# Kernel optimization log

Measured on AMD Instinct MI355X. Metric: run time of the kernel, lower is better.

Reference implementation:

```python
import jax, jax.numpy as jnp
import numpy as np

N = 100_000      # nodes
E = 3_200_000    # edges
H = 32           # hidden_dim
L = 4            # num_layers
G = 1_000        # graphs in batch
F_IN = 1         # num_features
C = 2            # num_classes
BN_EPS = 1e-5


def setup_inputs() -> dict:
    key = jax.random.key(0)
    ks = jax.random.split(key, 8)
    s = 0.1  # param init scale
    x = jax.random.normal(ks[0], (N, F_IN), jnp.float32)
    edge_index = jax.random.randint(ks[1], (2, E), 0, N, dtype=jnp.int64)
    batch = jnp.sort(jax.random.randint(ks[2], (N,), 0, G, dtype=jnp.int64))
    return {
        "x": x,
        "edge_index": edge_index,
        "batch": batch,
        "W_enc": jax.random.normal(ks[3], (F_IN, H), jnp.float32) * s,
        "b_enc": jnp.zeros((H,), jnp.float32),
        "eps": jnp.zeros((L,), jnp.float32),           # GIN train_eps, init 0
        "W1": jax.random.normal(ks[4], (L, H, H), jnp.float32) * s,
        "b1": jnp.zeros((L, H), jnp.float32),
        "W2": jax.random.normal(ks[5], (L, H, H), jnp.float32) * s,
        "b2": jnp.zeros((L, H), jnp.float32),
        "gamma": jnp.ones((L, H), jnp.float32),
        "beta": jnp.zeros((L, H), jnp.float32),
        "W_cls": jax.random.normal(ks[6], (H, C), jnp.float32) * s,
        "b_cls": jnp.zeros((C,), jnp.float32),
    }


def reference(x, edge_index, batch, W_enc, b_enc, eps, W1, b1, W2, b2,
              gamma, beta, W_cls, b_cls):
    h = x @ W_enc + b_enc                      # [N, H] node encoder
    src, dst = edge_index[0], edge_index[1]    # message flow src -> dst
    for l in range(L):
        # GINConv: (1+eps)*x + sum_{j in N(i)} x_j
        agg = jax.ops.segment_sum(h[src], dst, num_segments=N)   # [N, H]
        z = (1.0 + eps[l]) * h + agg
        # 2-layer MLP
        z = jnp.maximum(z @ W1[l] + b1[l], 0.0) @ W2[l] + b2[l]
        # BatchNorm1d (training-mode batch statistics over nodes)
        mu = z.mean(axis=0)
        var = z.var(axis=0)
        z = gamma[l] * (z - mu) * jax.lax.rsqrt(var + BN_EPS) + beta[l]
        h = jnp.maximum(z, 0.0)                # ReLU (dropout = identity, eval)
    pooled = jax.ops.segment_sum(h, batch, num_segments=G)   # global_add_pool
    return pooled @ W_cls + b_cls              # [G, C]
```

## Files before the change

kernel.cpp:

```cpp
#include <hip/hip_runtime.h>

#define N_NODES 100000
#define N_EDGES 3200000
#define HD      32
#define NLAYERS 4
#define NGRAPHS 1000
#define BN_EPS  1e-5f
#define BSHIFT  9
#define NBUCK   ((N_NODES + 511) >> 9)
#define PCHUNK  8192
#define NPB     ((N_EDGES + PCHUNK - 1) / PCHUNK)
#define ZBLOCKS ((NGRAPHS * HD + 255) / 256)

typedef _Float16 f16;
typedef _Float16 f16x8 __attribute__((ext_vector_type(8)));
typedef float    f32x4 __attribute__((ext_vector_type(4)));
typedef int      i32x4 __attribute__((ext_vector_type(4)));
typedef unsigned int  u32x2 __attribute__((ext_vector_type(2)));
typedef unsigned char uc8 __attribute__((ext_vector_type(8)));

__global__ __launch_bounds__(256) void k_encphist(
    const int* __restrict__ ei, float* __restrict__ stats,
    float* __restrict__ pooled, int* __restrict__ pcnt)
{
    __shared__ int hist[256];
    int bb = blockIdx.x, t = threadIdx.x;
    if (bb < NPB) {
        hist[t] = 0;
        __syncthreads();
        int base4 = bb * (PCHUNK / 4);
        int n4 = min(PCHUNK / 4, N_EDGES / 4 - base4);
        const i32x4* d4 = (const i32x4*)(ei + N_EDGES);
        for (int k = t; k < n4; k += 256) {
            i32x4 d = __builtin_nontemporal_load(d4 + base4 + k);
            atomicAdd(&hist[d.x >> BSHIFT], 1);
            atomicAdd(&hist[d.y >> BSHIFT], 1);
            atomicAdd(&hist[d.z >> BSHIFT], 1);
            atomicAdd(&hist[d.w >> BSHIFT], 1);
        }
        __syncthreads();
        pcnt[t * NPB + bb] = hist[t];
    } else {
        int gid = (bb - NPB) * 256 + t;
        if (gid < NLAYERS * 64)   stats[gid]  = 0.f;
        if (gid < NGRAPHS * HD)   pooled[gid] = 0.f;
    }
}

__global__ __launch_bounds__(512) void k_pscanA(int* __restrict__ pcnt,
                                                int* __restrict__ btot)
{
    __shared__ int sc[2][512];
    int t = threadIdx.x, b = blockIdx.x;
    int base = b * NPB;
    int v = (t < NPB) ? pcnt[base + t] : 0;
    int pp = 0;
    sc[0][t] = v;
    __syncthreads();
    for (int st = 1; st < 512; st <<= 1) {
        int x = sc[pp][t];
        if (t >= st) x += sc[pp][t - st];
        sc[pp ^ 1][t] = x;
        pp ^= 1;
        __syncthreads();
    }
    int incl = sc[pp][t];
    if (t < NPB) pcnt[base + t] = incl - v;
    if (t == NPB - 1) btot[b] = incl;
}

__global__ __launch_bounds__(256) void k_pscatter(const int* __restrict__ ei,
                                                  const int* __restrict__ pcnt,
                                                  const int* __restrict__ btot,
                                                  unsigned int* __restrict__ ebuf)
{
    __shared__ int sb[2][256];
    __shared__ int lcur[256];
    int t = threadIdx.x, blk = blockIdx.x;
    sb[0][t] = (t < NBUCK) ? btot[t] : 0;
    __syncthreads();
    int pp = 0;
    for (int st = 1; st < 256; st <<= 1) {
        int v = sb[pp][t];
        if (t >= st) v += sb[pp][t - st];
        sb[pp ^ 1][t] = v;
        pp ^= 1;
        __syncthreads();
    }
    int bexcl = (t == 0) ? 0 : sb[pp][t - 1];
    lcur[t] = pcnt[t * NPB + blk] + bexcl;
    __syncthreads();
    int base4 = blk * (PCHUNK / 4);
    int n4 = min(PCHUNK / 4, N_EDGES / 4 - base4);
    const i32x4* s4 = (const i32x4*)ei;
    const i32x4* d4 = (const i32x4*)(ei + N_EDGES);
    for (int k = t; k < n4; k += 256) {
        i32x4 s = __builtin_nontemporal_load(s4 + base4 + k);
        i32x4 d = __builtin_nontemporal_load(d4 + base4 + k);
        int pos;
        pos = atomicAdd(&lcur[d.x >> BSHIFT], 1);
        ebuf[pos] = ((unsigned)s.x << BSHIFT) | (unsigned)(d.x & 511);
        pos = atomicAdd(&lcur[d.y >> BSHIFT], 1);
        ebuf[pos] = ((unsigned)s.y << BSHIFT) | (unsigned)(d.y & 511);
        pos = atomicAdd(&lcur[d.z >> BSHIFT], 1);
        ebuf[pos] = ((unsigned)s.z << BSHIFT) | (unsigned)(d.z & 511);
        pos = atomicAdd(&lcur[d.w >> BSHIFT], 1);
        ebuf[pos] = ((unsigned)s.w << BSHIFT) | (unsigned)(d.w & 511);
    }
}

__global__ __launch_bounds__(512) void k_bfinal(const unsigned int* __restrict__ ebuf,
                                                const int* __restrict__ btot,
                                                const float* __restrict__ x,
                                                int* __restrict__ off,
                                                int* __restrict__ csr,
                                                float* __restrict__ usum)
{
    __shared__ int sb[2][256];
    __shared__ int cnt[512], scanbuf[2][512], cur[512];
    __shared__ float fsum[512];
    int tid = threadIdx.x, b = blockIdx.x;
    if (tid < 256) sb[0][tid] = (tid < NBUCK) ? btot[tid] : 0;
    fsum[tid] = 0.f;
    __syncthreads();
    int pp = 0;
    for (int st = 1; st < 256; st <<= 1) {
        if (tid < 256) {
            int v = sb[pp][tid];
            if (tid >= st) v += sb[pp][tid - st];
            sb[pp ^ 1][tid] = v;
        }
        pp ^= 1;
        __syncthreads();
    }
    int base = (b == 0) ? 0 : sb[pp][b - 1];
    int nE = sb[pp][b] - base;
    if (b == NBUCK - 1 && tid == 0) off[N_NODES] = sb[pp][NBUCK - 1];
    cnt[tid] = 0;
    __syncthreads();
    for (int e = tid; e < nE; e += 512)
        atomicAdd(&cnt[ebuf[base + e] & 511], 1);
    __syncthreads();
    int p2 = 0;
    scanbuf[0][tid] = cnt[tid];
    __syncthreads();
    for (int st = 1; st < 512; st <<= 1) {
        int v = scanbuf[p2][tid];
        if (tid >= st) v += scanbuf[p2][tid - st];
        scanbuf[p2 ^ 1][tid] = v;
        p2 ^= 1;
        __syncthreads();
    }
    int excl = scanbuf[p2][tid] - cnt[tid];
    cur[tid] = excl;
    int gnode = (b << BSHIFT) + tid;
    if (gnode < N_NODES) off[gnode] = base + excl;
    __syncthreads();
    for (int e = tid; e < nE; e += 512) {
        unsigned int p = ebuf[base + e];
        int src = (int)(p >> BSHIFT);
        int pos = atomicAdd(&cur[p & 511], 1);
        csr[base + pos] = src;
        atomicAdd(&fsum[p & 511], x[src]);
    }
    __syncthreads();
    if (gnode < N_NODES) usum[gnode] = fsum[tid];
}

__global__ __launch_bounds__(256, 6) void k_fused(
    const unsigned char* __restrict__ hq, const float* __restrict__ x,
    const float* __restrict__ usum, const int* __restrict__ off,
    const int* __restrict__ csr, const float* __restrict__ epsArr,
    const float* __restrict__ gamma, const float* __restrict__ beta,
    const float* __restrict__ W_enc, const float* __restrict__ b_enc,
    const float* __restrict__ W1, const float* __restrict__ b1,
    const float* __restrict__ W2, const float* __restrict__ b2,
    f16* __restrict__ z2out, float* __restrict__ stats, int layer)
{
    __shared__ f16 AT[4][16][5][8];
    __shared__ float T[4][16 * 36];
    __shared__ float redS[4][32], redQ[4][32];
    int tid = threadIdx.x, wave = tid >> 6, lane = tid & 63;
    int col = lane & 15, quad = lane >> 4;
    int unit = tid >> 2, li = tid & 3, ul = unit & 15;
    int node = blockIdx.x * 64 + unit;
    bool valid = node < N_NODES;
    int co = li * 8;

    f16x8 r;
    #pragma unroll
    for (int k = 0; k < 8; ++k) r[k] = (f16)0.f;

    if (valid) {
        if (layer == 0) {
            int j0 = off[node], jend = off[node + 1];
            float oneEps = 1.f + epsArr[0];
            float u  = fmaf(oneEps, x[node], usum[node]);
            float dv = oneEps + (float)(jend - j0);
            #pragma unroll
            for (int k = 0; k < 8; ++k)
                r[k] = (f16)(fmaf(u, W_enc[co + k], dv * b_enc[co + k]));
        } else {
            const unsigned MASK = 0x00FF00FFu;
            int j = off[node], jend = off[node + 1];
            u32x2 gs = *(const u32x2*)(hq + (size_t)node * 32 + co);
            unsigned a0 = 0, a1 = 0, a2 = 0, a3 = 0;
            auto accum = [&](u32x2 v) {
                a0 += v.x & MASK; a1 += (v.x >> 8) & MASK;
                a2 += v.y & MASK; a3 += (v.y >> 8) & MASK;
            };
            auto rowp = [&](int idx) {
                return (const u32x2*)(hq + (size_t)idx * 32 + co);
            };
            while (j < jend && (j & 3))
                accum(*rowp(csr[j++]));
            int nrem = jend - j;
            while (nrem >= 16) {
                i32x4 q0 = __builtin_nontemporal_load((const i32x4*)(csr + j));
                i32x4 q1 = __builtin_nontemporal_load((const i32x4*)(csr + j + 4));
                i32x4 q2 = __builtin_nontemporal_load((const i32x4*)(csr + j + 8));
                i32x4 q3 = __builtin_nontemporal_load((const i32x4*)(csr + j + 12));
                u32x2 g0 = *rowp(q0.x), g1 = *rowp(q0.y);
                u32x2 g2 = *rowp(q0.z), g3 = *rowp(q0.w);
                u32x2 g4 = *rowp(q1.x), g5 = *rowp(q1.y);
                u32x2 g6 = *rowp(q1.z), g7 = *rowp(q1.w);
                u32x2 g8 = *rowp(q2.x), g9 = *rowp(q2.y);
                u32x2 gA = *rowp(q2.z), gB = *rowp(q2.w);
                u32x2 gC = *rowp(q3.x), gD = *rowp(q3.y);
                u32x2 gE = *rowp(q3.z), gF = *rowp(q3.w);
                accum(g0); accum(g1); accum(g2); accum(g3);
                accum(g4); accum(g5); accum(g6); accum(g7);
                accum(g8); accum(g9); accum(gA); accum(gB);
                accum(gC); accum(gD); accum(gE); accum(gF);
                j += 16; nrem -= 16;
            }
            if (nrem >= 8) {
                i32x4 q0 = *(const i32x4*)(csr + j);
                i32x4 q1 = *(const i32x4*)(csr + j + 4);
                u32x2 g0 = *rowp(q0.x), g1 = *rowp(q0.y);
                u32x2 g2 = *rowp(q0.z), g3 = *rowp(q0.w);
                u32x2 g4 = *rowp(q1.x), g5 = *rowp(q1.y);
                u32x2 g6 = *rowp(q1.z), g7 = *rowp(q1.w);
                accum(g0); accum(g1); accum(g2); accum(g3);
                accum(g4); accum(g5); accum(g6); accum(g7);
                j += 8; nrem -= 8;
            }
            if (nrem >= 4) {
                i32x4 q0 = *(const i32x4*)(csr + j);
                accum(*rowp(q0.x)); accum(*rowp(q0.y));
                accum(*rowp(q0.z)); accum(*rowp(q0.w));
                j += 4;
            }
            while (j < jend)
                accum(*rowp(csr[j++]));

            float oneEps = 1.f + epsArr[layer];
            float F[8];
            F[0] = (float)(a0 & 0xFFFF); F[2] = (float)(a0 >> 16);
            F[1] = (float)(a1 & 0xFFFF); F[3] = (float)(a1 >> 16);
            F[4] = (float)(a2 & 0xFFFF); F[6] = (float)(a2 >> 16);
            F[5] = (float)(a3 & 0xFFFF); F[7] = (float)(a3 >> 16);
            #pragma unroll
            for (int k = 0; k < 4; ++k) {
                float gLo  = gamma[(layer - 1) * 32 + co + k];
                float bLo  = beta[(layer - 1) * 32 + co + k];
                float gHi  = gamma[(layer - 1) * 32 + co + k + 4];
                float bHi  = beta[(layer - 1) * 32 + co + k + 4];
                float sLo = fmaxf(fmaxf(bLo + 5.5f * fabsf(gLo), 0.f), 1e-6f) / 255.f;
                float sHi = fmaxf(fmaxf(bHi + 5.5f * fabsf(gHi), 0.f), 1e-6f) / 255.f;
                float qsl = (float)((gs.x >> (8 * k)) & 255u);
                float qsh = (float)((gs.y >> (8 * k)) & 255u);
                r[k]     = (f16)(sLo * (F[k]     + oneEps * qsl));
                r[k + 4] = (f16)(sHi * (F[k + 4] + oneEps * qsh));
            }
        }
    }

    if (valid) *(f16x8*)&AT[wave][ul][li][0] = r;

    float sA = 0.f, qA = 0.f, sB = 0.f, qB = 0.f;
    if (valid) {
        f16x8 a = *(const f16x8*)&AT[wave][col][quad][0];
        const float* W1l = W1 + layer * 1024;
        const float* W2l = W2 + layer * 1024;
        f16x8 w1a, w1b, w2a, w2b;
        #pragma unroll
        for (int jj = 0; jj < 8; ++jj) {
            int k = quad * 8 + jj;
            w1a[jj] = (f16)W1l[k * 32 + col];
            w1b[jj] = (f16)W1l[k * 32 + col + 16];
            w2a[jj] = (f16)W2l[k * 32 + col];
            w2b[jj] = (f16)W2l[k * 32 + col + 16];
        }
        float b1a = b1[layer * 32 + col], b1b = b1[layer * 32 + col + 16];
        float b2a = b2[layer * 32 + col], b2b = b2[layer * 32 + col + 16];
        f32x4 bias1a = {b1a, b1a, b1a, b1a}, bias1b = {b1b, b1b, b1b, b1b};
        f32x4 bias2a = {b2a, b2a, b2a, b2a}, bias2b = {b2b, b2b, b2b, b2b};
        float* Tw = T[wave];

        f32x4 m0 = __builtin_amdgcn_mfma_f32_16x16x32_f16(a, w1a, bias1a, 0, 0, 0);
        f32x4 m1 = __builtin_amdgcn_mfma_f32_16x16x32_f16(a, w1b, bias1b, 0, 0, 0);
        #pragma unroll
        for (int rr = 0; rr < 4; ++rr) {
            int row = quad * 4 + rr;
            Tw[row * 36 + col]      = fmaxf(m0[rr], 0.f);
            Tw[row * 36 + col + 16] = fmaxf(m1[rr], 0.f);
        }
        f32x4 t0 = *(const f32x4*)(Tw + col * 36 + quad * 8);
        f32x4 t1 = *(const f32x4*)(Tw + col * 36 + quad * 8 + 4);
        f16x8 a2;
        #pragma unroll
        for (int k = 0; k < 4; ++k) { a2[k] = (f16)t0[k]; a2[k + 4] = (f16)t1[k]; }
        f32x4 z0 = __builtin_amdgcn_mfma_f32_16x16x32_f16(a2, w2a, bias2a, 0, 0, 0);
        f32x4 zb = __builtin_amdgcn_mfma_f32_16x16x32_f16(a2, w2b, bias2b, 0, 0, 0);
        int nb = blockIdx.x * 64 + wave * 16;
        #pragma unroll
        for (int rr = 0; rr < 4; ++rr) {
            int n2 = nb + quad * 4 + rr;
            __builtin_nontemporal_store((f16)z0[rr], z2out + n2 * 32 + col);
            __builtin_nontemporal_store((f16)zb[rr], z2out + n2 * 32 + col + 16);
            sA += z0[rr]; qA += z0[rr] * z0[rr];
            sB += zb[rr]; qB += zb[rr] * zb[rr];
        }
    }

    sA += __shfl_xor(sA, 16); sA += __shfl_xor(sA, 32);
    qA += __shfl_xor(qA, 16); qA += __shfl_xor(qA, 32);
    sB += __shfl_xor(sB, 16); sB += __shfl_xor(sB, 32);
    qB += __shfl_xor(qB, 16); qB += __shfl_xor(qB, 32);
    if (lane < 16) {
        redS[wave][col] = sA; redS[wave][col + 16] = sB;
        redQ[wave][col] = qA; redQ[wave][col + 16] = qB;
    }
    __syncthreads();
    if (tid < 64) {
        int sel = tid >> 5, cc = tid & 31;
        float s = 0.f;
        #pragma unroll
        for (int w = 0; w < 4; ++w) s += sel ? redQ[w][cc] : redS[w][cc];
        atomicAdd(&stats[layer * 64 + sel * 32 + cc], s);
    }
}

__global__ __launch_bounds__(256) void k_quant(
    const f16* __restrict__ z2, const float* __restrict__ stats,
    const float* __restrict__ gamma, const float* __restrict__ beta,
    unsigned char* __restrict__ hq, int layer)
{
    int idx = blockIdx.x * 256 + threadIdx.x;
    if (idx >= N_NODES * 4) return;
    int c0 = (idx & 3) * 8;
    const float invN = 1.0f / (float)N_NODES;
    float bnsc[8], bnsh[8], inv_s[8];
    #pragma unroll
    for (int k = 0; k < 8; ++k) {
        int ch = c0 + k;
        float g = gamma[layer * 32 + ch], bb = beta[layer * 32 + ch];
        float mu  = stats[layer * 64 + ch] * invN;
        float var = stats[layer * 64 + 32 + ch] * invN - mu * mu;
        float sc = g * rsqrtf(var + BN_EPS);
        bnsc[k] = sc;
        bnsh[k] = bb - mu * sc;
        float vmax = fmaxf(bb + 5.5f * fabsf(g), 0.f);
        inv_s[k] = 255.f / fmaxf(vmax, 1e-6f);
    }
    f16x8 z = *(const f16x8*)(z2 + (size_t)idx * 8);
    uc8 r;
    #pragma unroll
    for (int k = 0; k < 8; ++k) {
        float v = fmaxf(fmaf((float)z[k], bnsc[k], bnsh[k]), 0.f);
        int q = (int)(fminf(v * inv_s[k], 255.f) + 0.5f);
        r[k] = (unsigned char)q;
    }
    __builtin_nontemporal_store(r, (uc8*)(hq + (size_t)idx * 8));
}

__global__ __launch_bounds__(256) void k_pool(const f16* __restrict__ z2,
                                              const int* __restrict__ batch,
                                              const float* __restrict__ stats,
                                              const float* __restrict__ gamma,
                                              const float* __restrict__ beta,
                                              float* __restrict__ pooled)
{
    int c = threadIdx.x & 31, slot = threadIdx.x >> 5;
    const float invN = 1.0f / (float)N_NODES;
    float mu  = stats[3 * 64 + c] * invN;
    float var = stats[3 * 64 + 32 + c] * invN - mu * mu;
    float sc = gamma[3 * 32 + c] * rsqrtf(var + BN_EPS);
    float sh = beta[3 * 32 + c] - mu * sc;
    int start = blockIdx.x * 256 + slot * 32;
    if (start >= N_NODES) return;
    int end = min(start + 32, N_NODES);
    int cur = batch[start]; float acc = 0.f;
    for (int i = start; i < end; ++i) {
        int g = batch[i];
        if (g != cur) { atomicAdd(&pooled[cur * HD + c], acc); acc = 0.f; cur = g; }
        acc += fmaxf(fmaf((float)z2[i * 32 + c], sc, sh), 0.f);
    }
    atomicAdd(&pooled[cur * HD + c], acc);
}

__global__ __launch_bounds__(256) void k_cls(const float* __restrict__ pooled,
                                             const float* __restrict__ Wc,
                                             const float* __restrict__ bc,
                                             float* __restrict__ out)
{
    int gid = blockIdx.x * 256 + threadIdx.x;
    if (gid >= NGRAPHS * 2) return;
    int g = gid >> 1, c = gid & 1;
    float s = bc[c];
    #pragma unroll
    for (int k = 0; k < 32; ++k) s = fmaf(pooled[g * 32 + k], Wc[k * 2 + c], s);
    out[gid] = s;
}

extern "C" void kernel_launch(void* const* d_in, const int* in_sizes, int n_in,
                              void* d_out, int out_size, void* d_ws, size_t ws_size,
                              hipStream_t stream)
{
    const float* x      = (const float*)d_in[0];
    const int*   ei     = (const int*)d_in[1];
    const int*   batch  = (const int*)d_in[2];
    const float* W_enc  = (const float*)d_in[3];
    const float* b_enc  = (const float*)d_in[4];
    const float* epsArr = (const float*)d_in[5];
    const float* W1     = (const float*)d_in[6];
    const float* b1     = (const float*)d_in[7];
    const float* W2     = (const float*)d_in[8];
    const float* b2     = (const float*)d_in[9];
    const float* gamma  = (const float*)d_in[10];
    const float* beta   = (const float*)d_in[11];
    const float* Wc     = (const float*)d_in[12];
    const float* bc     = (const float*)d_in[13];
    float* out = (float*)d_out;

    char* ws = (char*)d_ws;
    size_t o = 0;
    auto alloc = [&](size_t bytes) {
        char* p = ws + o;
        o += (bytes + 255) & ~(size_t)255;
        return p;
    };
    unsigned char* hq = (unsigned char*)alloc((size_t)N_NODES * 32);
    f16*   z2     = (f16*) alloc((size_t)N_NODES * 32 * 2);
    int*   csr    = (int*) alloc((size_t)N_EDGES * 4);
    unsigned int* ebuf = (unsigned int*)alloc((size_t)N_EDGES * 4);
    int*   offA   = (int*) alloc((size_t)(N_NODES + 1) * 4);
    float* usum   = (float*)alloc((size_t)N_NODES * 4);
    int*   pcnt   = (int*) alloc((size_t)256 * NPB * 4);
    int*   btot   = (int*) alloc(1024);
    float* stats  = (float*)alloc(NLAYERS * 64 * 4);
    float* pooled = (float*)alloc((size_t)NGRAPHS * HD * 4);

    k_encphist<<<NPB + ZBLOCKS, 256, 0, stream>>>(ei, stats, pooled, pcnt);
    k_pscanA  <<<NBUCK, 512, 0, stream>>>(pcnt, btot);
    k_pscatter<<<NPB, 256, 0, stream>>>(ei, pcnt, btot, ebuf);
    k_bfinal  <<<NBUCK, 512, 0, stream>>>(ebuf, btot, x, offA, csr, usum);

    for (int l = 0; l < NLAYERS; ++l) {
        k_fused<<<(N_NODES + 63) / 64, 256, 0, stream>>>(
            hq, x, usum, offA, csr, epsArr, gamma, beta, W_enc, b_enc,
            W1, b1, W2, b2, z2, stats, l);
        if (l < NLAYERS - 1)
            k_quant<<<(N_NODES * 4 + 255) / 256, 256, 0, stream>>>(z2, stats,
                                                                   gamma, beta,
                                                                   hq, l);
    }
    k_pool<<<(N_NODES + 255) / 256, 256, 0, stream>>>(z2, batch, stats,
                                                      gamma, beta, pooled);
    k_cls <<<8, 256, 0, stream>>>(pooled, Wc, bc, out);
}
```

Baseline: 443.2 us.

## Split fused gather across 8 lanes per node with shuffled CSR index loads

Doubles the block size of the fused GIN layer kernel to 512 threads so each node is gathered by 8 lanes of 4 bytes instead of 4 lanes of 8 bytes. The lanes of a node cooperatively load CSR indices (one per lane) and broadcast them with shuffles, and the next batch of indices is prefetched before the accumulation. The goal is more memory-level parallelism and fewer redundant index loads in the neighbor gather. Only the first four waves do the MFMA MLP, so half the block sits idle at that stage, and a block barrier is added before it.

```diff
diff --git a/kernel.cpp b/kernel.cpp
--- a/kernel.cpp
+++ b/kernel.cpp
@@ -13,6 +13,7 @@
 #define ZBLOCKS ((NGRAPHS * HD + 255) / 256)
 
 typedef _Float16 f16;
+typedef _Float16 f16x4 __attribute__((ext_vector_type(4)));
 typedef _Float16 f16x8 __attribute__((ext_vector_type(8)));
 typedef float    f32x4 __attribute__((ext_vector_type(4)));
 typedef int      i32x4 __attribute__((ext_vector_type(4)));
@@ -167,7 +168,7 @@
     if (gnode < N_NODES) usum[gnode] = fsum[tid];
 }
 
-__global__ __launch_bounds__(256, 6) void k_fused(
+__global__ __launch_bounds__(512, 8) void k_fused(
     const unsigned char* __restrict__ hq, const float* __restrict__ x,
     const float* __restrict__ usum, const int* __restrict__ off,
     const int* __restrict__ csr, const float* __restrict__ epsArr,
@@ -177,110 +178,91 @@
     const float* __restrict__ W2, const float* __restrict__ b2,
     f16* __restrict__ z2out, float* __restrict__ stats, int layer)
 {
-    __shared__ f16 AT[4][16][5][8];
+    __shared__ f16 AT[64][40];
     __shared__ float T[4][16 * 36];
     __shared__ float redS[4][32], redQ[4][32];
     int tid = threadIdx.x, wave = tid >> 6, lane = tid & 63;
-    int col = lane & 15, quad = lane >> 4;
-    int unit = tid >> 2, li = tid & 3, ul = unit & 15;
+    int unit = tid >> 3, li = tid & 7;
+    int lbase = lane & 56;
     int node = blockIdx.x * 64 + unit;
-    bool valid = node < N_NODES;
-    int co = li * 8;
-
-    f16x8 r;
-    #pragma unroll
-    for (int k = 0; k < 8; ++k) r[k] = (f16)0.f;
-
-    if (valid) {
+    int c0 = li * 4;
+
+    if (node < N_NODES) {
+        f16x4 r;
         if (layer == 0) {
-            int j0 = off[node], jend = off[node + 1];
             float oneEps = 1.f + epsArr[0];
             float u  = fmaf(oneEps, x[node], usum[node]);
-            float dv = oneEps + (float)(jend - j0);
+            float dv = oneEps + (float)(off[node + 1] - off[node]);
             #pragma unroll
-            for (int k = 0; k < 8; ++k)
-                r[k] = (f16)(fmaf(u, W_enc[co + k], dv * b_enc[co + k]));
+            for (int k = 0; k < 4; ++k)
+                r[k] = (f16)(fmaf(u, W_enc[c0 + k], dv * b_enc[c0 + k]));
         } else {
             const unsigned MASK = 0x00FF00FFu;
+            const unsigned char* hql = hq + c0;
             int j = off[node], jend = off[node + 1];
-            u32x2 gs = *(const u32x2*)(hq + (size_t)node * 32 + co);
-            unsigned a0 = 0, a1 = 0, a2 = 0, a3 = 0;
-            auto accum = [&](u32x2 v) {
-                a0 += v.x & MASK; a1 += (v.x >> 8) & MASK;
-                a2 += v.y & MASK; a3 += (v.y >> 8) & MASK;
-            };
-            auto rowp = [&](int idx) {
-                return (const u32x2*)(hq + (size_t)idx * 32 + co);
-            };
-            while (j < jend && (j & 3))
-                accum(*rowp(csr[j++]));
-            int nrem = jend - j;
-            while (nrem >= 16) {
-                i32x4 q0 = __builtin_nontemporal_load((const i32x4*)(csr + j));
-                i32x4 q1 = __builtin_nontemporal_load((const i32x4*)(csr + j + 4));
-                i32x4 q2 = __builtin_nontemporal_load((const i32x4*)(csr + j + 8));
-                i32x4 q3 = __builtin_nontemporal_load((const i32x4*)(csr + j + 12));
-                u32x2 g0 = *rowp(q0.x), g1 = *rowp(q0.y);
-                u32x2 g2 = *rowp(q0.z), g3 = *rowp(q0.w);
-                u32x2 g4 = *rowp(q1.x), g5 = *rowp(q1.y);
-                u32x2 g6 = *rowp(q1.z), g7 = *rowp(q1.w);
-                u32x2 g8 = *rowp(q2.x), g9 = *rowp(q2.y);
-                u32x2 gA = *rowp(q2.z), gB = *rowp(q2.w);
-                u32x2 gC = *rowp(q3.x), gD = *rowp(q3.y);
-                u32x2 gE = *rowp(q3.z), gF = *rowp(q3.w);
-                accum(g0); accum(g1); accum(g2); accum(g3);
-                accum(g4); accum(g5); accum(g6); accum(g7);
-                accum(g8); accum(g9); accum(gA); accum(gB);
-                accum(gC); accum(gD); accum(gE); accum(gF);
-                j += 16; nrem -= 16;
+            int navail = jend - j;
+            unsigned qv = *(const unsigned*)(hql + (size_t)node * 32);
+            int ci0 = 0, ci1 = 0;
+            if (li < navail)     ci0 = __builtin_nontemporal_load(csr + j + li);
+            if (8 + li < navail) ci1 = __builtin_nontemporal_load(csr + j + 8 + li);
+            unsigned a0 = 0, a1 = 0;
+            while (navail >= 16) {
+                unsigned g[16];
+                #pragma unroll
+                for (int e = 0; e < 8; ++e) {
+                    int i0 = __shfl(ci0, lbase | e);
+                    int i1 = __shfl(ci1, lbase | e);
+                    g[e]     = *(const unsigned*)(hql + (size_t)i0 * 32);
+                    g[e + 8] = *(const unsigned*)(hql + (size_t)i1 * 32);
+                }
+                j += 16; navail -= 16;
+                if (li < navail)     ci0 = __builtin_nontemporal_load(csr + j + li);
+                if (8 + li < navail) ci1 = __builtin_nontemporal_load(csr + j + 8 + li);
+                #pragma unroll
+                for (int e = 0; e < 16; ++e) {
+                    a0 += g[e] & MASK; a1 += (g[e] >> 8) & MASK;
+                }
             }
-            if (nrem >= 8) {
-                i32x4 q0 = *(const i32x4*)(csr + j);
-                i32x4 q1 = *(const i32x4*)(csr + j + 4);
-                u32x2 g0 = *rowp(q0.x), g1 = *rowp(q0.y);
-                u32x2 g2 = *rowp(q0.z), g3 = *rowp(q0.w);
-                u32x2 g4 = *rowp(q1.x), g5 = *rowp(q1.y);
-                u32x2 g6 = *rowp(q1.z), g7 = *rowp(q1.w);
-                accum(g0); accum(g1); accum(g2); accum(g3);
-                accum(g4); accum(g5); accum(g6); accum(g7);
-                j += 8; nrem -= 8;
+            if (navail >= 8) {
+                unsigned g[8];
+                #pragma unroll
+                for (int e = 0; e < 8; ++e) {
+                    int i0 = __shfl(ci0, lbase | e);
+                    g[e] = *(const unsigned*)(hql + (size_t)i0 * 32);
+                }
+                ci0 = ci1; j += 8; navail -= 8;
+                #pragma unroll
+                for (int e = 0; e < 8; ++e) {
+                    a0 += g[e] & MASK; a1 += (g[e] >> 8) & MASK;
+                }
             }
-            if (nrem >= 4) {
-                i32x4 q0 = *(const i32x4*)(csr + j);
-                accum(*rowp(q0.x)); accum(*rowp(q0.y));
-                accum(*rowp(q0.z)); accum(*rowp(q0.w));
-                j += 4;
+            for (int e = 0; e < navail; ++e) {
+                int i0 = __shfl(ci0, lbase | e);
+                unsigned g = *(const unsigned*)(hql + (size_t)i0 * 32);
+                a0 += g & MASK; a1 += (g >> 8) & MASK;
             }
-            while (j < jend)
-                accum(*rowp(csr[j++]));
-
             float oneEps = 1.f + epsArr[layer];
-            float F[8];
+            float F[4];
             F[0] = (float)(a0 & 0xFFFF); F[2] = (float)(a0 >> 16);
             F[1] = (float)(a1 & 0xFFFF); F[3] = (float)(a1 >> 16);
-            F[4] = (float)(a2 & 0xFFFF); F[6] = (float)(a2 >> 16);
-            F[5] = (float)(a3 & 0xFFFF); F[7] = (float)(a3 >> 16);
             #pragma unroll
             for (int k = 0; k < 4; ++k) {
-                float gLo  = gamma[(layer - 1) * 32 + co + k];
-                float bLo  = beta[(layer - 1) * 32 + co + k];
-                float gHi  = gamma[(layer - 1) * 32 + co + k + 4];
-                float bHi  = beta[(layer - 1) * 32 + co + k + 4];
-                float sLo = fmaxf(fmaxf(bLo + 5.5f * fabsf(gLo), 0.f), 1e-6f) / 255.f;
-                float sHi = fmaxf(fmaxf(bHi + 5.5f * fabsf(gHi), 0.f), 1e-6f) / 255.f;
-                float qsl = (float)((gs.x >> (8 * k)) & 255u);
-                float qsh = (float)((gs.y >> (8 * k)) & 255u);
-                r[k]     = (f16)(sLo * (F[k]     + oneEps * qsl));
-                r[k + 4] = (f16)(sHi * (F[k + 4] + oneEps * qsh));
+                float g  = gamma[(layer - 1) * 32 + c0 + k];
+                float bb = beta[(layer - 1) * 32 + c0 + k];
+                float s  = fmaxf(fmaxf(bb + 5.5f * fabsf(g), 0.f), 1e-6f) / 255.f;
+                float q  = (float)((qv >> (8 * k)) & 255u);
+                r[k] = (f16)(s * (F[k] + oneEps * q));
             }
         }
-    }
-
-    if (valid) *(f16x8*)&AT[wave][ul][li][0] = r;
-
+        *(f16x4*)&AT[unit][c0] = r;
+    }
+    __syncthreads();
+
+    int col = lane & 15, quad = lane >> 4;
     float sA = 0.f, qA = 0.f, sB = 0.f, qB = 0.f;
-    if (valid) {
-        f16x8 a = *(const f16x8*)&AT[wave][col][quad][0];
+    int nb = blockIdx.x * 64 + wave * 16;
+    if (wave < 4 && nb < N_NODES) {
+        f16x8 a = *(const f16x8*)&AT[wave * 16 + col][quad * 8];
         const float* W1l = W1 + layer * 1024;
         const float* W2l = W2 + layer * 1024;
         f16x8 w1a, w1b, w2a, w2b;
@@ -313,7 +295,6 @@
         for (int k = 0; k < 4; ++k) { a2[k] = (f16)t0[k]; a2[k + 4] = (f16)t1[k]; }
         f32x4 z0 = __builtin_amdgcn_mfma_f32_16x16x32_f16(a2, w2a, bias2a, 0, 0, 0);
         f32x4 zb = __builtin_amdgcn_mfma_f32_16x16x32_f16(a2, w2b, bias2b, 0, 0, 0);
-        int nb = blockIdx.x * 64 + wave * 16;
         #pragma unroll
         for (int rr = 0; rr < 4; ++rr) {
             int n2 = nb + quad * 4 + rr;
@@ -323,14 +304,15 @@
             sB += zb[rr]; qB += zb[rr] * zb[rr];
         }
     }
-
-    sA += __shfl_xor(sA, 16); sA += __shfl_xor(sA, 32);
-    qA += __shfl_xor(qA, 16); qA += __shfl_xor(qA, 32);
-    sB += __shfl_xor(sB, 16); sB += __shfl_xor(sB, 32);
-    qB += __shfl_xor(qB, 16); qB += __shfl_xor(qB, 32);
-    if (lane < 16) {
-        redS[wave][col] = sA; redS[wave][col + 16] = sB;
-        redQ[wave][col] = qA; redQ[wave][col + 16] = qB;
+    if (wave < 4) {
+        sA += __shfl_xor(sA, 16); sA += __shfl_xor(sA, 32);
+        qA += __shfl_xor(qA, 16); qA += __shfl_xor(qA, 32);
+        sB += __shfl_xor(sB, 16); sB += __shfl_xor(sB, 32);
+        qB += __shfl_xor(qB, 16); qB += __shfl_xor(qB, 32);
+        if (lane < 16) {
+            redS[wave][col] = sA; redS[wave][col + 16] = sB;
+            redQ[wave][col] = qA; redQ[wave][col + 16] = qB;
+        }
     }
     __syncthreads();
     if (tid < 64) {
@@ -458,7 +440,7 @@
     k_bfinal  <<<NBUCK, 512, 0, stream>>>(ebuf, btot, x, offA, csr, usum);
 
     for (int l = 0; l < NLAYERS; ++l) {
-        k_fused<<<(N_NODES + 63) / 64, 256, 0, stream>>>(
+        k_fused<<<(N_NODES + 63) / 64, 512, 0, stream>>>(
             hq, x, usum, offA, csr, epsArr, gamma, beta, W_enc, b_enc,
             W1, b1, W2, b2, z2, stats, l);
         if (l < NLAYERS - 1)
```

After: 419.1 us. -5.4%, faster.
